# Kernel tuning notes

Hardware: AMD Instinct MI355X
Metric: run time of the kernel (lower is better)

The kernel has to match this reference:

```python
import jax, jax.numpy as jnp
import numpy as np

B, L, D_FEAT = 16, 2048, 512
H, D_HID, UNITS = 8, 512, 512


def setup_inputs() -> dict:
    key = jax.random.key(0)
    ks = jax.random.split(key, 8)
    s_feat = 1.0 / np.sqrt(D_FEAT)
    s_hid = 1.0 / np.sqrt(D_HID)
    s_u = 1.0 / np.sqrt(UNITS)
    return {
        "features": jax.random.normal(ks[0], (B, L, D_FEAT), jnp.float32),
        "hidden": jax.random.normal(ks[1], (B, H, D_HID), jnp.float32),
        # Per-head Dense params stacked along a leading head axis.
        "W1": jax.random.normal(ks[2], (H, D_FEAT, UNITS), jnp.float32) * s_feat,
        "b1": jnp.zeros((H, UNITS), jnp.float32),
        "W2": jax.random.normal(ks[3], (H, D_HID, UNITS), jnp.float32) * s_hid,
        "b2": jnp.zeros((H, UNITS), jnp.float32),
        "V": jax.random.normal(ks[4], (H, UNITS), jnp.float32) * s_u,
        "bV": jnp.zeros((H,), jnp.float32),
    }


def reference(features, hidden, W1, b1, W2, b2, V, bV):
    # features: [B, L, Df]; hidden: [B, H, Dh]
    # Per-head: tanh(W1(features) + W2(hidden_h)) -> V -> softmax over L -> weighted sum.
    f_proj = jnp.einsum("bld,hdu->bhlu", features, W1) + b1[None, :, None, :]   # [B,H,L,U]
    h_proj = jnp.einsum("bhd,hdu->bhu", hidden, W2) + b2[None, :, :]            # [B,H,U]
    act = jnp.tanh(f_proj + h_proj[:, :, None, :])                               # [B,H,L,U]
    score = jnp.einsum("bhlu,hu->bhl", act, V) + bV[None, :, None]               # [B,H,L]
    attn = jax.nn.softmax(score, axis=-1)                                        # softmax over L
    context = jnp.einsum("bhl,bld->bhd", attn, features)                         # [B,H,Df]
    # Original stacks weights (each [B,L,1]) along axis=2 -> [B,L,H,1]
    attention_weights = jnp.transpose(attn, (0, 2, 1))[..., None]                # [B,L,H,1]
    return context, attention_weights
```

## Files before the change

### kernel.cpp

```cpp
#include <hip/hip_runtime.h>
#include <hip/hip_bf16.h>

#define B_ 16
#define L_ 2048
#define DF 512
#define H_ 8
#define DH 512
#define U_ 512

typedef unsigned short u16;
typedef __attribute__((ext_vector_type(8))) short bf16x8;
typedef __attribute__((ext_vector_type(4))) float f32x4;

__device__ __forceinline__ u16 f2bf(float x) {
  __hip_bfloat16 h = __float2bfloat16(x);
  u16 u;
  __builtin_memcpy(&u, &h, 2);
  return u;
}

__device__ __forceinline__ void load_lds16(const void* g, void* l) {
  __builtin_amdgcn_global_load_lds(
      (const __attribute__((address_space(1))) void*)g,
      (__attribute__((address_space(3))) void*)l, 16, 0, 0);
}

__device__ __forceinline__ float fast_tanh2(float x) {
  float e = __expf(2.f * x);
  return 1.f - __fdividef(2.f, e + 1.f);
}

__global__ __launch_bounds__(256) void prep_kernel(
    const float* __restrict__ F, u16* __restrict__ Abf,
    const float* __restrict__ W1, u16* __restrict__ W1T,
    const float* __restrict__ hidden, const float* __restrict__ W2,
    float* __restrict__ hpart) {
  __shared__ float t[32][33];
  __shared__ float hs[B_][64];
  if (blockIdx.x < 16384) {
    size_t i = ((size_t)blockIdx.x * 256 + threadIdx.x) * 4;
    float4 v = *(const float4*)(F + i);
    ushort4 o;
    o.x = f2bf(v.x); o.y = f2bf(v.y); o.z = f2bf(v.z); o.w = f2bf(v.w);
    *(ushort4*)(Abf + i) = o;
  } else if (blockIdx.x < 18432) {
    int bid = blockIdx.x - 16384;
    int d0 = (bid & 15) * 32, u0 = ((bid >> 4) & 15) * 32, h = bid >> 8;
    const float* src = W1 + (size_t)h * DF * U_;
    u16* dst = W1T + (size_t)h * U_ * DF;
#pragma unroll
    for (int i = 0; i < 4; ++i) {
      int idx = threadIdx.x + i * 256;
      int r = idx >> 5, c = idx & 31;
      t[r][c] = src[(size_t)(d0 + r) * U_ + u0 + c];
    }
    __syncthreads();
#pragma unroll
    for (int i = 0; i < 4; ++i) {
      int idx = threadIdx.x + i * 256;
      int r = idx >> 5, c = idx & 31;
      dst[(size_t)(u0 + r) * DF + d0 + c] = f2bf(t[c][r]);
    }
  } else {
    int bid = blockIdx.x - 18432;
    int h = bid & 7, uy = (bid >> 3) & 1, dz = bid >> 4;
    int u = uy * 256 + threadIdx.x;
    int d0 = dz * 64;
    for (int idx = threadIdx.x; idx < B_ * 64; idx += 256) {
      int b = idx >> 6, d = idx & 63;
      hs[b][d] = hidden[(size_t)(b * H_ + h) * DH + d0 + d];
    }
    __syncthreads();
    float acc[B_];
#pragma unroll
    for (int b = 0; b < B_; b++) acc[b] = 0.f;
    const float* w2p = W2 + ((size_t)h * DH + d0) * U_ + u;
    for (int d = 0; d < 64; d++) {
      float w = w2p[(size_t)d * U_];
#pragma unroll
      for (int b = 0; b < B_; b++) acc[b] += hs[b][d] * w;
    }
#pragma unroll
    for (int b = 0; b < B_; b++)
      hpart[(((size_t)dz * B_ + b) * H_ + h) * U_ + u] = acc[b];
  }
}

__global__ __launch_bounds__(256) void hproj_combine_kernel(
    const float* __restrict__ partial, const float* __restrict__ b1,
    const float* __restrict__ b2, float* __restrict__ c) {
  int i = blockIdx.x * 256 + threadIdx.x;
  int hu = i & (H_ * U_ - 1);
  float s = b1[hu] + b2[hu];
#pragma unroll
  for (int z = 0; z < 8; z++) s += partial[(size_t)z * B_ * H_ * U_ + i];
  c[i] = s;
}

#define BKS 64

__global__ __launch_bounds__(512, 4) void score_kernel(
    const u16* __restrict__ Abf, const u16* __restrict__ W1T,
    const float* __restrict__ C, const float* __restrict__ V,
    float* __restrict__ score) {
  int l0 = blockIdx.x * 128;
  int b = blockIdx.y, h = blockIdx.z;
  int tid = threadIdx.x;
  int lane = tid & 63, wid = tid >> 6;
  int wr = wid >> 2, wc = wid & 3;
  int rl = lane & 15;
  int q = lane >> 4;
  int khalf = q << 3;

  __shared__ u16 As[2][128 * BKS];
  __shared__ u16 Bs[2][128 * BKS];
  __shared__ float redsm[4][128];

  const u16* Fb = Abf + (size_t)b * L_ * DF;
  const u16* Wh = W1T + (size_t)h * U_ * DF;
  const float* Cb = C + (size_t)(b * H_ + h) * U_;
  const float* Vh = V + (size_t)h * U_;

  float part[16];
#pragma unroll
  for (int p = 0; p < 16; ++p) part[p] = 0.f;

#define STAGE(buf, kbase)                                                  \
  {                                                                        \
    _Pragma("unroll") for (int i_ = 0; i_ < 2; ++i_) {                     \
      int idx_ = i_ * 512 + tid;                                           \
      int row_ = idx_ >> 3;                                                \
      int ke_ = ((idx_ & 7) ^ (row_ & 7)) << 3;                            \
      load_lds16(Fb + (((size_t)(l0 + row_)) << 9) + (kbase) + ke_,        \
                 &As[buf][idx_ * 8]);                                      \
      load_lds16(Wh + (((size_t)(N0 + row_)) << 9) + (kbase) + ke_,        \
                 &Bs[buf][idx_ * 8]);                                      \
    }                                                                      \
  }

  for (int nc = 0; nc < 4; ++nc) {
    int N0 = nc * 128;
    float cu[2], vv[2];
#pragma unroll
    for (int n = 0; n < 2; ++n) {
      int col = N0 + wc * 32 + n * 16 + rl;
      cu[n] = Cb[col];
      vv[n] = Vh[col];
    }
    f32x4 acc[4][2];
#pragma unroll
    for (int m = 0; m < 4; ++m)
#pragma unroll
      for (int n = 0; n < 2; ++n)
#pragma unroll
        for (int j = 0; j < 4; ++j) acc[m][n][j] = cu[n];

    STAGE(0, 0);
    int cur = 0;
    for (int kt = 0; kt < 8; ++kt) {
      if (kt < 7) {
        STAGE(cur ^ 1, (kt + 1) * BKS);
        asm volatile("s_waitcnt vmcnt(4)" ::: "memory");
      } else {
        asm volatile("s_waitcnt vmcnt(0)" ::: "memory");
      }
      __builtin_amdgcn_s_barrier();
#pragma unroll
      for (int s = 0; s < 2; ++s) {
        bf16x8 bfr[2];
#pragma unroll
        for (int n = 0; n < 2; ++n) {
          int rB = wc * 32 + n * 16 + rl;
          bfr[n] = *(const bf16x8*)&Bs[cur][(rB << 6) +
                                            ((s * 32 + khalf) ^
                                             ((rB & 7) << 3))];
        }
#pragma unroll
        for (int m = 0; m < 4; ++m) {
          int rA = wr * 64 + m * 16 + rl;
          bf16x8 af = *(const bf16x8*)&As[cur][(rA << 6) +
                                               ((s * 32 + khalf) ^
                                                ((rA & 7) << 3))];
#pragma unroll
          for (int n = 0; n < 2; ++n)
            acc[m][n] = __builtin_amdgcn_mfma_f32_16x16x32_bf16(
                af, bfr[n], acc[m][n], 0, 0, 0);
        }
      }
      asm volatile("s_waitcnt lgkmcnt(0)" ::: "memory");
      __builtin_amdgcn_s_barrier();
      cur ^= 1;
    }
#pragma unroll
    for (int n = 0; n < 2; ++n)
#pragma unroll
      for (int m = 0; m < 4; ++m)
#pragma unroll
        for (int j = 0; j < 4; ++j)
          part[m * 4 + j] += fast_tanh2(acc[m][n][j]) * vv[n];
  }
#undef STAGE

#pragma unroll
  for (int p = 0; p < 16; ++p) {
    float v = part[p];
    v += __shfl_xor(v, 1, 64);
    v += __shfl_xor(v, 2, 64);
    v += __shfl_xor(v, 4, 64);
    v += __shfl_xor(v, 8, 64);
    part[p] = v;
  }
  __syncthreads();
  if (rl == 0) {
#pragma unroll
    for (int m = 0; m < 4; ++m)
#pragma unroll
      for (int j = 0; j < 4; ++j)
        redsm[wc][wr * 64 + m * 16 + q * 4 + j] = part[m * 4 + j];
  }
  __syncthreads();
  if (tid < 128) {
    float s = redsm[0][tid] + redsm[1][tid] + redsm[2][tid] + redsm[3][tid];
    score[(size_t)(b * H_ + h) * L_ + l0 + tid] = s;
  }
}

__global__ __launch_bounds__(256) void softmax_kernel(
    const float* __restrict__ score, float* __restrict__ attn,
    float* __restrict__ aw_out) {
  int bh = blockIdx.x;
  int b = bh / H_, h = bh % H_;
  const float* s = score + (size_t)bh * L_;
  __shared__ float sv[L_];
  __shared__ float red[256];

  for (int i = threadIdx.x; i < L_ / 4; i += 256)
    ((float4*)sv)[i] = ((const float4*)s)[i];
  __syncthreads();

  float m = -1e30f;
  for (int l = threadIdx.x; l < L_; l += 256) m = fmaxf(m, sv[l]);
  red[threadIdx.x] = m;
  __syncthreads();
  for (int st = 128; st > 0; st >>= 1) {
    if (threadIdx.x < st)
      red[threadIdx.x] = fmaxf(red[threadIdx.x], red[threadIdx.x + st]);
    __syncthreads();
  }
  m = red[0];
  __syncthreads();

  float sum = 0.f;
  for (int l = threadIdx.x; l < L_; l += 256) sum += __expf(sv[l] - m);
  red[threadIdx.x] = sum;
  __syncthreads();
  for (int st = 128; st > 0; st >>= 1) {
    if (threadIdx.x < st) red[threadIdx.x] += red[threadIdx.x + st];
    __syncthreads();
  }
  float inv = 1.f / red[0];

  for (int l = threadIdx.x; l < L_; l += 256) {
    float a = __expf(sv[l] - m) * inv;
    attn[(size_t)bh * L_ + l] = a;
    aw_out[((size_t)b * L_ + l) * H_ + h] = a;
  }
}

__global__ __launch_bounds__(256) void context_part_kernel(
    const float* __restrict__ F, const float* __restrict__ attn,
    float* __restrict__ partial) {
  int b = blockIdx.x;
  int d0 = blockIdx.y * 64;
  int lz = blockIdx.z;
  int td = threadIdx.x & 63;
  int tl = threadIdx.x >> 6;

  __shared__ float as[H_][256];
  for (int idx = threadIdx.x; idx < H_ * 256; idx += 256)
    as[idx >> 8][idx & 255] =
        attn[((size_t)b * H_ + (idx >> 8)) * L_ + lz * 256 + (idx & 255)];
  __syncthreads();

  float acc[H_] = {};
  for (int l = tl; l < 256; l += 4) {
    float f = F[((size_t)b * L_ + lz * 256 + l) * DF + d0 + td];
#pragma unroll
    for (int h = 0; h < H_; h++) acc[h] += as[h][l] * f;
  }

  __shared__ float red[4][H_][64];
#pragma unroll
  for (int h = 0; h < H_; h++) red[tl][h][td] = acc[h];
  __syncthreads();
  if (tl == 0) {
#pragma unroll
    for (int h = 0; h < H_; h++) {
      float v = red[0][h][td] + red[1][h][td] + red[2][h][td] + red[3][h][td];
      partial[(size_t)lz * B_ * H_ * DF + ((size_t)b * H_ + h) * DF + d0 + td] =
          v;
    }
  }
}

__global__ __launch_bounds__(256) void context_combine_kernel(
    const float* __restrict__ partial, float* __restrict__ ctx_out) {
  int i = blockIdx.x * 256 + threadIdx.x;
  float s = 0.f;
#pragma unroll
  for (int z = 0; z < 8; z++) s += partial[(size_t)z * B_ * H_ * DF + i];
  ctx_out[i] = s;
}

extern "C" void kernel_launch(void* const* d_in, const int* in_sizes, int n_in,
                              void* d_out, int out_size, void* d_ws,
                              size_t ws_size, hipStream_t stream) {
  const float* features = (const float*)d_in[0];
  const float* hidden   = (const float*)d_in[1];
  const float* W1       = (const float*)d_in[2];
  const float* b1       = (const float*)d_in[3];
  const float* W2       = (const float*)d_in[4];
  const float* b2       = (const float*)d_in[5];
  const float* V        = (const float*)d_in[6];

  float* out = (float*)d_out;
  float* ctx_out = out;
  float* aw_out  = out + B_ * H_ * DF;

  float* c_buf = (float*)d_ws;
  float* score = c_buf + (size_t)B_ * H_ * U_;
  float* attn  = score;
  float* hpart = score;
  float* cpart = score + (size_t)B_ * H_ * L_;
  u16* Abf = (u16*)(cpart + (size_t)8 * B_ * H_ * DF);
  u16* W1T = Abf + (size_t)B_ * L_ * DF;

  prep_kernel<<<16384 + 2048 + 128, 256, 0, stream>>>(features, Abf, W1, W1T,
                                                      hidden, W2, hpart);
  hproj_combine_kernel<<<(B_ * H_ * U_) / 256, 256, 0, stream>>>(hpart, b1, b2,
                                                                 c_buf);
  score_kernel<<<dim3(L_ / 128, B_, H_), 512, 0, stream>>>(Abf, W1T, c_buf, V,
                                                           score);
  softmax_kernel<<<B_ * H_, 256, 0, stream>>>(score, attn, aw_out);
  context_part_kernel<<<dim3(B_, DF / 64, 8), 256, 0, stream>>>(features, attn,
                                                                cpart);
  context_combine_kernel<<<(B_ * H_ * DF) / 256, 256, 0, stream>>>(cpart,
                                                                   ctx_out);
}
```

Baseline: 240.5 us.

## Enlarge score GEMM tile to 256x256 with 1024 threads; read bf16 features in context

The score kernel now computes 256x256 output tiles with 16 waves per block, each wave holding a 64x64 accumulator. The two N-chunks run as one flattened 16-step double-buffered pipeline, with the tanh·V reduction done at the chunk boundary. The aim is to raise arithmetic intensity and cut redundant global/LDS reloads of the A and W1 tiles. Separately, the context kernel reads the bf16 copy of features instead of fp32, halving its memory traffic at some precision cost. The larger tile uses 128KB LDS and more registers per thread, which reduces occupancy, and the declared launch bound of 4 blocks may not be achievable.

```diff
diff --git a/kernel.cpp b/kernel.cpp
--- a/kernel.cpp
+++ b/kernel.cpp
@@ -17,6 +17,13 @@
   u16 u;
   __builtin_memcpy(&u, &h, 2);
   return u;
+}
+
+__device__ __forceinline__ float bf2f(u16 u) {
+  unsigned x = ((unsigned)u) << 16;
+  float f;
+  __builtin_memcpy(&f, &x, 4);
+  return f;
 }
 
 __device__ __forceinline__ void load_lds16(const void* g, void* l) {
@@ -97,109 +104,124 @@
   c[i] = s;
 }
 
-#define BKS 64
-
-__global__ __launch_bounds__(512, 4) void score_kernel(
+#define BKV 64
+
+__global__ __launch_bounds__(1024, 4) void score_kernel(
     const u16* __restrict__ Abf, const u16* __restrict__ W1T,
     const float* __restrict__ C, const float* __restrict__ V,
     float* __restrict__ score) {
-  int l0 = blockIdx.x * 128;
+  int l0 = blockIdx.x * 256;
   int b = blockIdx.y, h = blockIdx.z;
   int tid = threadIdx.x;
   int lane = tid & 63, wid = tid >> 6;
   int wr = wid >> 2, wc = wid & 3;
-  int rl = lane & 15;
-  int q = lane >> 4;
+  int rl = lane & 15, q = lane >> 4;
   int khalf = q << 3;
 
-  __shared__ u16 As[2][128 * BKS];
-  __shared__ u16 Bs[2][128 * BKS];
-  __shared__ float redsm[4][128];
-
-  const u16* Fb = Abf + (size_t)b * L_ * DF;
+  __shared__ u16 As[2][256 * BKV];
+  __shared__ u16 Bs[2][256 * BKV];
+  __shared__ float redsm[4][256];
+
+  const u16* Fb = Abf + ((size_t)b * L_ + l0) * DF;
   const u16* Wh = W1T + (size_t)h * U_ * DF;
   const float* Cb = C + (size_t)(b * H_ + h) * U_;
   const float* Vh = V + (size_t)h * U_;
 
+  float cu[2][4], vv[2][4];
+#pragma unroll
+  for (int nc = 0; nc < 2; ++nc)
+#pragma unroll
+    for (int n = 0; n < 4; ++n) {
+      int col = nc * 256 + wc * 64 + n * 16 + rl;
+      cu[nc][n] = Cb[col];
+      vv[nc][n] = Vh[col];
+    }
+
   float part[16];
 #pragma unroll
   for (int p = 0; p < 16; ++p) part[p] = 0.f;
 
-#define STAGE(buf, kbase)                                                  \
+  f32x4 acc[4][4];
+#pragma unroll
+  for (int m = 0; m < 4; ++m)
+#pragma unroll
+    for (int n = 0; n < 4; ++n)
+#pragma unroll
+      for (int j = 0; j < 4; ++j) acc[m][n][j] = cu[0][n];
+
+#define STAGE(buf, kb, N0)                                                 \
   {                                                                        \
     _Pragma("unroll") for (int i_ = 0; i_ < 2; ++i_) {                     \
-      int idx_ = i_ * 512 + tid;                                           \
+      int idx_ = i_ * 1024 + tid;                                          \
       int row_ = idx_ >> 3;                                                \
       int ke_ = ((idx_ & 7) ^ (row_ & 7)) << 3;                            \
-      load_lds16(Fb + (((size_t)(l0 + row_)) << 9) + (kbase) + ke_,        \
+      load_lds16(Fb + ((size_t)row_ << 9) + (kb) + ke_,                    \
                  &As[buf][idx_ * 8]);                                      \
-      load_lds16(Wh + (((size_t)(N0 + row_)) << 9) + (kbase) + ke_,        \
+      load_lds16(Wh + (((size_t)((N0) + row_)) << 9) + (kb) + ke_,         \
                  &Bs[buf][idx_ * 8]);                                      \
     }                                                                      \
   }
 
-  for (int nc = 0; nc < 4; ++nc) {
-    int N0 = nc * 128;
-    float cu[2], vv[2];
-#pragma unroll
-    for (int n = 0; n < 2; ++n) {
-      int col = N0 + wc * 32 + n * 16 + rl;
-      cu[n] = Cb[col];
-      vv[n] = Vh[col];
-    }
-    f32x4 acc[4][2];
+#define COMPUTE(bufi)                                                      \
+  {                                                                        \
+    _Pragma("unroll") for (int ss = 0; ss < 2; ++ss) {                     \
+      bf16x8 bF[4];                                                        \
+      _Pragma("unroll") for (int n = 0; n < 4; ++n) {                      \
+        int rB = wc * 64 + n * 16 + rl;                                    \
+        bF[n] = *(const bf16x8*)&Bs[bufi][(rB << 6) +                      \
+                                          ((ss * 32 + khalf) ^             \
+                                           ((rB & 7) << 3))];              \
+      }                                                                    \
+      _Pragma("unroll") for (int m = 0; m < 4; ++m) {                      \
+        int rA = wr * 64 + m * 16 + rl;                                    \
+        bf16x8 aF = *(const bf16x8*)&As[bufi][(rA << 6) +                  \
+                                             ((ss * 32 + khalf) ^          \
+                                              ((rA & 7) << 3))];           \
+        _Pragma("unroll") for (int n = 0; n < 4; ++n)                      \
+          acc[m][n] = __builtin_amdgcn_mfma_f32_16x16x32_bf16(             \
+              aF, bF[n], acc[m][n], 0, 0, 0);                              \
+      }                                                                    \
+    }                                                                      \
+  }
+
+  STAGE(0, 0, 0);
+
+#pragma unroll 1
+  for (int s = 0; s < 16; ++s) {
+    int cur = s & 1;
+    if (s < 15) {
+      int kb = ((s + 1) & 7) * BKV;
+      int N0n = ((s + 1) >> 3) * 256;
+      STAGE(cur ^ 1, kb, N0n);
+      asm volatile("s_waitcnt vmcnt(4)" ::: "memory");
+    } else {
+      asm volatile("s_waitcnt vmcnt(0)" ::: "memory");
+    }
+    __builtin_amdgcn_s_barrier();
+    COMPUTE(cur);
+    if (s == 7) {
+#pragma unroll
+      for (int n = 0; n < 4; ++n)
+#pragma unroll
+        for (int m = 0; m < 4; ++m)
+#pragma unroll
+          for (int j = 0; j < 4; ++j) {
+            part[m * 4 + j] += fast_tanh2(acc[m][n][j]) * vv[0][n];
+            acc[m][n][j] = cu[1][n];
+          }
+    }
+    asm volatile("s_waitcnt lgkmcnt(0)" ::: "memory");
+    __builtin_amdgcn_s_barrier();
+  }
+#pragma unroll
+  for (int n = 0; n < 4; ++n)
 #pragma unroll
     for (int m = 0; m < 4; ++m)
 #pragma unroll
-      for (int n = 0; n < 2; ++n)
-#pragma unroll
-        for (int j = 0; j < 4; ++j) acc[m][n][j] = cu[n];
-
-    STAGE(0, 0);
-    int cur = 0;
-    for (int kt = 0; kt < 8; ++kt) {
-      if (kt < 7) {
-        STAGE(cur ^ 1, (kt + 1) * BKS);
-        asm volatile("s_waitcnt vmcnt(4)" ::: "memory");
-      } else {
-        asm volatile("s_waitcnt vmcnt(0)" ::: "memory");
-      }
-      __builtin_amdgcn_s_barrier();
-#pragma unroll
-      for (int s = 0; s < 2; ++s) {
-        bf16x8 bfr[2];
-#pragma unroll
-        for (int n = 0; n < 2; ++n) {
-          int rB = wc * 32 + n * 16 + rl;
-          bfr[n] = *(const bf16x8*)&Bs[cur][(rB << 6) +
-                                            ((s * 32 + khalf) ^
-                                             ((rB & 7) << 3))];
-        }
-#pragma unroll
-        for (int m = 0; m < 4; ++m) {
-          int rA = wr * 64 + m * 16 + rl;
-          bf16x8 af = *(const bf16x8*)&As[cur][(rA << 6) +
-                                               ((s * 32 + khalf) ^
-                                                ((rA & 7) << 3))];
-#pragma unroll
-          for (int n = 0; n < 2; ++n)
-            acc[m][n] = __builtin_amdgcn_mfma_f32_16x16x32_bf16(
-                af, bfr[n], acc[m][n], 0, 0, 0);
-        }
-      }
-      asm volatile("s_waitcnt lgkmcnt(0)" ::: "memory");
-      __builtin_amdgcn_s_barrier();
-      cur ^= 1;
-    }
-#pragma unroll
-    for (int n = 0; n < 2; ++n)
-#pragma unroll
-      for (int m = 0; m < 4; ++m)
-#pragma unroll
-        for (int j = 0; j < 4; ++j)
-          part[m * 4 + j] += fast_tanh2(acc[m][n][j]) * vv[n];
-  }
+      for (int j = 0; j < 4; ++j)
+        part[m * 4 + j] += fast_tanh2(acc[m][n][j]) * vv[1][n];
 #undef STAGE
+#undef COMPUTE
 
 #pragma unroll
   for (int p = 0; p < 16; ++p) {
@@ -219,7 +241,7 @@
         redsm[wc][wr * 64 + m * 16 + q * 4 + j] = part[m * 4 + j];
   }
   __syncthreads();
-  if (tid < 128) {
+  if (tid < 256) {
     float s = redsm[0][tid] + redsm[1][tid] + redsm[2][tid] + redsm[3][tid];
     score[(size_t)(b * H_ + h) * L_ + l0 + tid] = s;
   }
@@ -268,7 +290,7 @@
 }
 
 __global__ __launch_bounds__(256) void context_part_kernel(
-    const float* __restrict__ F, const float* __restrict__ attn,
+    const u16* __restrict__ Abf, const float* __restrict__ attn,
     float* __restrict__ partial) {
   int b = blockIdx.x;
   int d0 = blockIdx.y * 64;
@@ -284,7 +306,7 @@
 
   float acc[H_] = {};
   for (int l = tl; l < 256; l += 4) {
-    float f = F[((size_t)b * L_ + lz * 256 + l) * DF + d0 + td];
+    float f = bf2f(Abf[((size_t)b * L_ + lz * 256 + l) * DF + d0 + td]);
 #pragma unroll
     for (int h = 0; h < H_; h++) acc[h] += as[h][l] * f;
   }
@@ -339,10 +361,10 @@
                                                       hidden, W2, hpart);
   hproj_combine_kernel<<<(B_ * H_ * U_) / 256, 256, 0, stream>>>(hpart, b1, b2,
                                                                  c_buf);
-  score_kernel<<<dim3(L_ / 128, B_, H_), 512, 0, stream>>>(Abf, W1T, c_buf, V,
-                                                           score);
+  score_kernel<<<dim3(L_ / 256, B_, H_), 1024, 0, stream>>>(Abf, W1T, c_buf, V,
+                                                            score);
   softmax_kernel<<<B_ * H_, 256, 0, stream>>>(score, attn, aw_out);
-  context_part_kernel<<<dim3(B_, DF / 64, 8), 256, 0, stream>>>(features, attn,
+  context_part_kernel<<<dim3(B_, DF / 64, 8), 256, 0, stream>>>(Abf, attn,
                                                                 cpart);
   context_combine_kernel<<<(B_ * H_ * DF) / 256, 256, 0, stream>>>(cpart,
                                                                    ctx_out);
```

Result: slower. 267.5 us (+11.2%).
